# Performance work log

Hardware: AMD Instinct MI355X
Metric: run time of the kernel (lower is better)

## Reference

```python
import jax, jax.numpy as jnp
import numpy as np


def setup_inputs() -> dict:
    key = jax.random.key(0)
    k1, k2, k3, k4 = jax.random.split(key, 4)
    B, T, F_in, F_out, N, E, K = 16, 64, 64, 64, 128, 2, 4
    x = jax.random.normal(k1, (B, T, F_in, N), dtype=jnp.float32)
    # graph shift operator per (batch, time, edge-feature); scaled to keep powers bounded
    S = jax.random.normal(k2, (B, T, E, N, N), dtype=jnp.float32) / np.sqrt(N)
    H = jax.random.normal(k3, (F_out, E, K, F_in), dtype=jnp.float32) * 0.02
    bias = jax.random.normal(k4, (F_out, 1), dtype=jnp.float32) * 0.02
    return {"x": x, "S": S, "H": H, "bias": bias}


def reference(x, S, H, bias):
    # x: [B,T,F_in,N], S: [B,T,E,N,N], H: [F_out,E,K,F_in], bias: [F_out,1]
    B, T, F_in, N = x.shape
    E = S.shape[2]
    F_out, _, K, _ = H.shape
    # replicate features across edge-feature dim: [B,T,E,F_in,N]
    cur = jnp.broadcast_to(x[:, :, None], (B, T, E, F_in, N))
    taps = [cur]
    zero_row = jnp.zeros((B, 1, E, F_in, N), dtype=x.dtype)
    for _ in range(1, K):
        # time-shift: tap k at time t depends on tap k-1 at time t-1
        cur = jnp.concatenate([zero_row, cur[:, :-1]], axis=1)
        # diffuse over graph: [..,F_in,N] @ [..,N,N]
        cur = jnp.matmul(cur, S)
        taps.append(cur)
    z = jnp.stack(taps, axis=2)  # [B,T,K,E,F_in,N]
    # [B,T,N, E*K*F_in], matching permute(0,1,5,3,2,4) in the source
    z = z.transpose(0, 1, 5, 3, 2, 4).reshape(B, T, N, E * K * F_in)
    Hm = H.reshape(F_out, E * K * F_in)
    y = jnp.einsum('btnf,of->bton', z, Hm)  # [B,T,F_out,N]
    return y + bias  # bias [F_out,1] broadcasts over N
```

## Files before the change

kernel.cpp:

```cpp
#include <hip/hip_runtime.h>


namespace {
constexpr int B = 16, T = 64, F = 64, N = 128, E = 2, K = 4;
constexpr int SH = 72;
constexpr int SX = 72;
constexpr int SA = 136;
}

typedef short v8s __attribute__((ext_vector_type(8)));
typedef float v4f __attribute__((ext_vector_type(4)));

__device__ inline ushort f2bf(float f) {
  union { float f; uint u; } v; v.f = f;
  uint u = v.u;
  return (ushort)((u + 0x7fffu + ((u >> 16) & 1u)) >> 16);
}

__device__ inline uint4 pack8(const ushort* p) {
  uint4 w;
  w.x = (uint)p[0] | ((uint)p[1] << 16);
  w.y = (uint)p[2] | ((uint)p[3] << 16);
  w.z = (uint)p[4] | ((uint)p[5] << 16);
  w.w = (uint)p[6] | ((uint)p[7] << 16);
  return w;
}

__global__ __launch_bounds__(256) void cvt_S(const float* __restrict__ S,
                                             ushort* __restrict__ ST,
                                             int e_base, int e_count) {
  __shared__ ushort tile[128 * 130];
  const int bid = blockIdx.x;
  const int le = bid % e_count, s = (bid / e_count) % T, b = bid / (e_count * T);
  const int e = e_base + le;
  const float* Sg = S + (size_t)((b * T + s) * E + e) * N * N;
  ushort* Og = ST + (size_t)((b * T + s) * e_count + le) * N * N;
  const int tid = threadIdx.x;
  #pragma unroll
  for (int it = 0; it < 16; ++it) {
    const int idx = tid + it * 256;
    const int m = idx >> 5, n4 = (idx & 31) * 4;
    const float4 v = *(const float4*)(Sg + m * N + n4);
    uint* lp = (uint*)&tile[m * 130 + n4];
    lp[0] = (uint)f2bf(v.x) | ((uint)f2bf(v.y) << 16);
    lp[1] = (uint)f2bf(v.z) | ((uint)f2bf(v.w) << 16);
  }
  __syncthreads();
  #pragma unroll
  for (int it = 0; it < 4; ++it) {
    const int idx = tid + it * 256;
    const int m8 = (idx & 15) * 8, n2 = idx >> 4;
    uint r[8];
    #pragma unroll
    for (int j = 0; j < 8; ++j)
      r[j] = *(const uint*)&tile[(m8 + j) * 130 + 2 * n2];
    uint4 w0, w1;
    w0.x = (r[0] & 0xffffu) | (r[1] << 16);
    w0.y = (r[2] & 0xffffu) | (r[3] << 16);
    w0.z = (r[4] & 0xffffu) | (r[5] << 16);
    w0.w = (r[6] & 0xffffu) | (r[7] << 16);
    w1.x = (r[0] >> 16) | (r[1] & 0xffff0000u);
    w1.y = (r[2] >> 16) | (r[3] & 0xffff0000u);
    w1.z = (r[4] >> 16) | (r[5] & 0xffff0000u);
    w1.w = (r[6] >> 16) | (r[7] & 0xffff0000u);
    *(uint4*)(Og + (2 * n2) * N + m8) = w0;
    *(uint4*)(Og + (2 * n2 + 1) * N + m8) = w1;
  }
}

__device__ inline void stage_H(const float* __restrict__ Hg, int e, int k,
                               ushort* sH, int tid) {
  #pragma unroll
  for (int it = 0; it < 2; ++it) {
    const int idx = tid + it * 256;
    const int o = idx & 63, f8 = (idx >> 6) * 8;
    const float* src = Hg + ((size_t)(o * E + e) * K + k) * F + f8;
    ushort p[8];
    #pragma unroll
    for (int j = 0; j < 8; ++j) p[j] = f2bf(src[j]);
    *(uint4*)&sH[o * SH + f8] = pack8(p);
  }
}

__device__ inline void stage_X(const float* __restrict__ xg, ushort* sX, int tid) {
  #pragma unroll
  for (int it = 0; it < 4; ++it) {
    const int idx = tid + it * 256;
    const int n = idx & 127, f8 = (idx >> 7) * 8;
    ushort p[8];
    #pragma unroll
    for (int j = 0; j < 8; ++j) p[j] = f2bf(xg[(f8 + j) * N + n]);
    *(uint4*)&sX[n * SX + f8] = pack8(p);
  }
}

__device__ inline void stage_A(const ushort* __restrict__ Pg, ushort* sA, int tid) {
  #pragma unroll
  for (int it = 0; it < 4; ++it) {
    const int idx = tid + it * 256;
    const int o = idx >> 4, m8 = (idx & 15) * 8;
    *(uint4*)&sA[o * SA + m8] = *(const uint4*)(Pg + o * N + m8);
  }
}

__device__ inline void stage_Sh(const ushort* __restrict__ STg, int h,
                                ushort* sB, int tid) {
  #pragma unroll
  for (int it = 0; it < 4; ++it) {
    const int idx = tid + it * 256;
    const int n = idx >> 3, m8 = (idx & 7) * 8;
    *(uint4*)&sB[n * SX + m8] = *(const uint4*)(STg + n * N + h * 64 + m8);
  }
}

__device__ inline void zero_acc(v4f acc[2][4]) {
  #pragma unroll
  for (int i = 0; i < 2; ++i)
    #pragma unroll
    for (int j = 0; j < 4; ++j) {
      acc[i][j][0] = 0.f; acc[i][j][1] = 0.f; acc[i][j][2] = 0.f; acc[i][j][3] = 0.f;
    }
}

__device__ inline void do_proj(const ushort* sH, const ushort* sX, v4f acc[2][4],
                               int ob0, int nb0, int l15, int q) {
  #pragma unroll
  for (int fk = 0; fk < 2; ++fk) {
    v8s a[2], bb[4];
    #pragma unroll
    for (int mt = 0; mt < 2; ++mt)
      a[mt] = *(const v8s*)&sH[(ob0 + 16 * mt + l15) * SH + fk * 32 + q * 8];
    #pragma unroll
    for (int nt = 0; nt < 4; ++nt)
      bb[nt] = *(const v8s*)&sX[(nb0 + 16 * nt + l15) * SX + fk * 32 + q * 8];
    #pragma unroll
    for (int mt = 0; mt < 2; ++mt)
      #pragma unroll
      for (int nt = 0; nt < 4; ++nt)
        acc[mt][nt] = __builtin_amdgcn_mfma_f32_16x16x32_bf16(
            a[mt], bb[nt], acc[mt][nt], 0, 0, 0);
  }
}

__device__ inline void do_mm(const ushort* sA, const ushort* sB, int h,
                             v4f acc[2][4], int ob0, int nb0, int l15, int q) {
  #pragma unroll
  for (int lk = 0; lk < 2; ++lk) {
    v8s a[2], bb[4];
    #pragma unroll
    for (int mt = 0; mt < 2; ++mt)
      a[mt] = *(const v8s*)&sA[(ob0 + 16 * mt + l15) * SA + h * 64 + lk * 32 + q * 8];
    #pragma unroll
    for (int nt = 0; nt < 4; ++nt)
      bb[nt] = *(const v8s*)&sB[(nb0 + 16 * nt + l15) * SX + lk * 32 + q * 8];
    #pragma unroll
    for (int mt = 0; mt < 2; ++mt)
      #pragma unroll
      for (int nt = 0; nt < 4; ++nt)
        acc[mt][nt] = __builtin_amdgcn_mfma_f32_16x16x32_bf16(
            a[mt], bb[nt], acc[mt][nt], 0, 0, 0);
  }
}

__device__ inline void store_W(ushort* __restrict__ Wg, v4f acc[2][4],
                               int ob0, int nb0, int l15, int q) {
  #pragma unroll
  for (int mt = 0; mt < 2; ++mt)
    #pragma unroll
    for (int nt = 0; nt < 4; ++nt) {
      const int col = nb0 + 16 * nt + l15;
      #pragma unroll
      for (int r = 0; r < 4; ++r)
        Wg[(ob0 + 16 * mt + q * 4 + r) * N + col] = f2bf(acc[mt][nt][r]);
    }
}

__device__ inline void store_sA(ushort* sA, v4f acc[2][4],
                                int ob0, int nb0, int l15, int q) {
  #pragma unroll
  for (int mt = 0; mt < 2; ++mt)
    #pragma unroll
    for (int nt = 0; nt < 4; ++nt) {
      const int col = nb0 + 16 * nt + l15;
      #pragma unroll
      for (int r = 0; r < 4; ++r)
        sA[(ob0 + 16 * mt + q * 4 + r) * SA + col] = f2bf(acc[mt][nt][r]);
    }
}

__global__ __launch_bounds__(256) void gf_p2(
    const float* __restrict__ x, const ushort* __restrict__ ST,
    const float* __restrict__ H, ushort* __restrict__ Out,
    int e_base, int e_count) {
  __shared__ ushort sH[64 * SH];
  __shared__ ushort sB[128 * SX];
  __shared__ ushort sA[64 * SA];
  const int bid = blockIdx.x;
  const int le = bid % e_count, s = (bid / e_count) % T, b = bid / (e_count * T);
  const int e = e_base + le;
  const int tid = threadIdx.x, w = tid >> 6, lane = tid & 63;
  const int l15 = lane & 15, q = lane >> 4;
  const int ob0 = (w & 1) * 32, nb0 = (w >> 1) * 64;
  const bool has_p = (s > 0);
  const ushort* STg = ST + (size_t)((b * T + s) * e_count + le) * N * N;
  v4f acc[2][4];
  zero_acc(acc);
  if (has_p) {
    stage_H(H, e, 3, sH, tid);
    stage_X(x + (size_t)(b * T + s - 1) * F * N, sB, tid);
    __syncthreads();
    do_proj(sH, sB, acc, ob0, nb0, l15, q);
    __syncthreads();
    store_sA(sA, acc, ob0, nb0, l15, q);
    zero_acc(acc);
  }
  stage_H(H, e, 2, sH, tid);
  stage_X(x + (size_t)(b * T + s) * F * N, sB, tid);
  __syncthreads();
  do_proj(sH, sB, acc, ob0, nb0, l15, q);
  if (has_p) {
    #pragma unroll
    for (int h = 0; h < 2; ++h) {
      __syncthreads();
      stage_Sh(STg, h, sB, tid);
      __syncthreads();
      do_mm(sA, sB, h, acc, ob0, nb0, l15, q);
    }
  }
  store_W(Out + (size_t)((b * T + s) * e_count + le) * F * N, acc, ob0, nb0, l15, q);
}

__global__ __launch_bounds__(256) void gf_p1(
    const float* __restrict__ x, const ushort* __restrict__ ST,
    const float* __restrict__ H, const ushort* __restrict__ Pin,
    ushort* __restrict__ Out, int ktap, int e_base, int e_count) {
  __shared__ ushort sH[64 * SH];
  __shared__ ushort sB[128 * SX];
  __shared__ ushort sA[64 * SA];
  const int bid = blockIdx.x;
  const int le = bid % e_count, s = (bid / e_count) % T, b = bid / (e_count * T);
  const int e = e_base + le;
  const int tid = threadIdx.x, w = tid >> 6, lane = tid & 63;
  const int l15 = lane & 15, q = lane >> 4;
  const int ob0 = (w & 1) * 32, nb0 = (w >> 1) * 64;
  const bool has_p = (s > 0);
  const ushort* STg = ST + (size_t)((b * T + s) * e_count + le) * N * N;
  v4f acc[2][4];
  zero_acc(acc);
  stage_H(H, e, ktap, sH, tid);
  stage_X(x + (size_t)(b * T + s) * F * N, sB, tid);
  if (has_p)
    stage_A(Pin + (size_t)((b * T + s - 1) * e_count + le) * F * N, sA, tid);
  __syncthreads();
  do_proj(sH, sB, acc, ob0, nb0, l15, q);
  if (has_p) {
    #pragma unroll
    for (int h = 0; h < 2; ++h) {
      __syncthreads();
      stage_Sh(STg, h, sB, tid);
      __syncthreads();
      do_mm(sA, sB, h, acc, ob0, nb0, l15, q);
    }
  }
  store_W(Out + (size_t)((b * T + s) * e_count + le) * F * N, acc, ob0, nb0, l15, q);
}

__global__ __launch_bounds__(256) void gf_final(
    const float* __restrict__ x, const ushort* __restrict__ ST,
    const float* __restrict__ H, const float* __restrict__ bias,
    const ushort* __restrict__ Pin, float* __restrict__ y,
    int e_base, int e_count, int first_pass) {
  __shared__ ushort sH[64 * SH];
  __shared__ ushort sB[128 * SX];
  __shared__ ushort sA[64 * SA];
  const int bid = blockIdx.x;
  const int t = bid % T, b = bid / T;
  const int tid = threadIdx.x, w = tid >> 6, lane = tid & 63;
  const int l15 = lane & 15, q = lane >> 4;
  const int ob0 = (w & 1) * 32, nb0 = (w >> 1) * 64;
  const bool has_p = (t > 0);
  v4f acc[2][4];
  zero_acc(acc);
  for (int le = 0; le < e_count; ++le) {
    const int e = e_base + le;
    __syncthreads();
    stage_H(H, e, 0, sH, tid);
    stage_X(x + (size_t)(b * T + t) * F * N, sB, tid);
    if (has_p)
      stage_A(Pin + (size_t)((b * T + t - 1) * e_count + le) * F * N, sA, tid);
    __syncthreads();
    do_proj(sH, sB, acc, ob0, nb0, l15, q);
    if (has_p) {
      const ushort* STg = ST + (size_t)((b * T + t) * e_count + le) * N * N;
      #pragma unroll
      for (int h = 0; h < 2; ++h) {
        __syncthreads();
        stage_Sh(STg, h, sB, tid);
        __syncthreads();
        do_mm(sA, sB, h, acc, ob0, nb0, l15, q);
      }
    }
  }
  float* yg = y + (size_t)(b * T + t) * F * N;
  #pragma unroll
  for (int mt = 0; mt < 2; ++mt)
    #pragma unroll
    for (int nt = 0; nt < 4; ++nt) {
      const int col = nb0 + 16 * nt + l15;
      #pragma unroll
      for (int r = 0; r < 4; ++r) {
        const int row = ob0 + 16 * mt + q * 4 + r;
        float v = acc[mt][nt][r];
        v += first_pass ? bias[row] : yg[row * N + col];
        yg[row * N + col] = v;
      }
    }
}

extern "C" void kernel_launch(void* const* d_in, const int* in_sizes, int n_in,
                              void* d_out, int out_size, void* d_ws, size_t ws_size,
                              hipStream_t stream) {
  const float* x    = (const float*)d_in[0];
  const float* S    = (const float*)d_in[1];
  const float* H    = (const float*)d_in[2];
  const float* bias = (const float*)d_in[3];
  float* y = (float*)d_out;

  const size_t ST2 = (size_t)B * T * 2 * N * N;
  const size_t W2e = (size_t)B * T * 2 * F * N;
  const size_t need2 = (ST2 + 2 * W2e) * sizeof(ushort);

  if (ws_size >= need2) {
    ushort* ST   = (ushort*)d_ws;
    ushort* bufA = ST + ST2;
    ushort* bufB = bufA + W2e;
    cvt_S   <<<B * T * 2, 256, 0, stream>>>(S, ST, 0, 2);
    gf_p2   <<<B * T * 2, 256, 0, stream>>>(x, ST, H, bufA, 0, 2);
    gf_p1   <<<B * T * 2, 256, 0, stream>>>(x, ST, H, bufA, bufB, 1, 0, 2);
    gf_final<<<B * T,     256, 0, stream>>>(x, ST, H, bias, bufB, y, 0, 2, 1);
  } else {
    const size_t ST1 = (size_t)B * T * N * N;
    const size_t W1e = (size_t)B * T * F * N;
    ushort* ST   = (ushort*)d_ws;
    ushort* bufA = ST + ST1;
    ushort* bufB = bufA + W1e;
    for (int e = 0; e < E; ++e) {
      cvt_S   <<<B * T, 256, 0, stream>>>(S, ST, e, 1);
      gf_p2   <<<B * T, 256, 0, stream>>>(x, ST, H, bufA, e, 1);
      gf_p1   <<<B * T, 256, 0, stream>>>(x, ST, H, bufA, bufB, 1, e, 1);
      gf_final<<<B * T, 256, 0, stream>>>(x, ST, H, bias, bufB, y, e, 1, e == 0);
    }
  }
}
```

Before: 321.6 us.

## Fuse the three Horner-style filter passes into one kernel per output step

Replaces the p2/p1/final kernel chain with a single fused kernel in which each (b,t) block recomputes the chain for all taps and both edge features, keeping intermediates in shared memory and registers instead of writing bf16 buffers to global memory. H is converted to bf16 once by a small pre-kernel. This removes the intermediate global round-trips and two launches, but each block now redoes the projections for previous time steps and runs serially over both edge features with fewer blocks (B*T instead of B*T*2), which lowers parallelism.

```diff
diff --git a/kernel.cpp b/kernel.cpp
--- a/kernel.cpp
+++ b/kernel.cpp
@@ -26,15 +26,24 @@
   return w;
 }
 
+__global__ __launch_bounds__(256) void cvt_H(const float* __restrict__ H,
+                                             ushort* __restrict__ Hb) {
+  const int d4 = blockIdx.x * 256 + threadIdx.x;
+  const int d = d4 * 4;
+  const int f = d & 63, o = (d >> 6) & 63, k = (d >> 12) & 3, e = (d >> 14) & 1;
+  const float4 v = *(const float4*)(H + (((size_t)o * E + e) * K + k) * F + f);
+  uint2 w;
+  w.x = (uint)f2bf(v.x) | ((uint)f2bf(v.y) << 16);
+  w.y = (uint)f2bf(v.z) | ((uint)f2bf(v.w) << 16);
+  *(uint2*)(Hb + d) = w;
+}
+
 __global__ __launch_bounds__(256) void cvt_S(const float* __restrict__ S,
-                                             ushort* __restrict__ ST,
-                                             int e_base, int e_count) {
+                                             ushort* __restrict__ ST) {
   __shared__ ushort tile[128 * 130];
   const int bid = blockIdx.x;
-  const int le = bid % e_count, s = (bid / e_count) % T, b = bid / (e_count * T);
-  const int e = e_base + le;
-  const float* Sg = S + (size_t)((b * T + s) * E + e) * N * N;
-  ushort* Og = ST + (size_t)((b * T + s) * e_count + le) * N * N;
+  const float* Sg = S + (size_t)bid * N * N;
+  ushort* Og = ST + (size_t)bid * N * N;
   const int tid = threadIdx.x;
   #pragma unroll
   for (int it = 0; it < 16; ++it) {
@@ -68,21 +77,18 @@
   }
 }
 
-__device__ inline void stage_H(const float* __restrict__ Hg, int e, int k,
-                               ushort* sH, int tid) {
+__device__ inline void stage_Hb(const ushort* __restrict__ Hb, int e, int k,
+                                ushort* sH, int tid) {
+  const ushort* src = Hb + (size_t)((e * K + k) * 64) * 64;
   #pragma unroll
   for (int it = 0; it < 2; ++it) {
     const int idx = tid + it * 256;
-    const int o = idx & 63, f8 = (idx >> 6) * 8;
-    const float* src = Hg + ((size_t)(o * E + e) * K + k) * F + f8;
-    ushort p[8];
-    #pragma unroll
-    for (int j = 0; j < 8; ++j) p[j] = f2bf(src[j]);
-    *(uint4*)&sH[o * SH + f8] = pack8(p);
-  }
-}
-
-__device__ inline void stage_X(const float* __restrict__ xg, ushort* sX, int tid) {
+    const int o = idx >> 3, f8 = (idx & 7) * 8;
+    *(uint4*)&sH[o * SH + f8] = *(const uint4*)(src + o * 64 + f8);
+  }
+}
+
+__device__ inline void stage_X(const float* __restrict__ xg, ushort* sB, int tid) {
   #pragma unroll
   for (int it = 0; it < 4; ++it) {
     const int idx = tid + it * 256;
@@ -90,16 +96,7 @@
     ushort p[8];
     #pragma unroll
     for (int j = 0; j < 8; ++j) p[j] = f2bf(xg[(f8 + j) * N + n]);
-    *(uint4*)&sX[n * SX + f8] = pack8(p);
-  }
-}
-
-__device__ inline void stage_A(const ushort* __restrict__ Pg, ushort* sA, int tid) {
-  #pragma unroll
-  for (int it = 0; it < 4; ++it) {
-    const int idx = tid + it * 256;
-    const int o = idx >> 4, m8 = (idx & 15) * 8;
-    *(uint4*)&sA[o * SA + m8] = *(const uint4*)(Pg + o * N + m8);
+    *(uint4*)&sB[n * SX + f8] = pack8(p);
   }
 }
 
@@ -122,7 +119,7 @@
     }
 }
 
-__device__ inline void do_proj(const ushort* sH, const ushort* sX, v4f acc[2][4],
+__device__ inline void do_proj(const ushort* sH, const ushort* sB, v4f acc[2][4],
                                int ob0, int nb0, int l15, int q) {
   #pragma unroll
   for (int fk = 0; fk < 2; ++fk) {
@@ -132,7 +129,7 @@
       a[mt] = *(const v8s*)&sH[(ob0 + 16 * mt + l15) * SH + fk * 32 + q * 8];
     #pragma unroll
     for (int nt = 0; nt < 4; ++nt)
-      bb[nt] = *(const v8s*)&sX[(nb0 + 16 * nt + l15) * SX + fk * 32 + q * 8];
+      bb[nt] = *(const v8s*)&sB[(nb0 + 16 * nt + l15) * SX + fk * 32 + q * 8];
     #pragma unroll
     for (int mt = 0; mt < 2; ++mt)
       #pragma unroll
@@ -162,8 +159,8 @@
   }
 }
 
-__device__ inline void store_W(ushort* __restrict__ Wg, v4f acc[2][4],
-                               int ob0, int nb0, int l15, int q) {
+__device__ inline void store_sA(ushort* sA, v4f acc[2][4],
+                                int ob0, int nb0, int l15, int q) {
   #pragma unroll
   for (int mt = 0; mt < 2; ++mt)
     #pragma unroll
@@ -171,105 +168,14 @@
       const int col = nb0 + 16 * nt + l15;
       #pragma unroll
       for (int r = 0; r < 4; ++r)
-        Wg[(ob0 + 16 * mt + q * 4 + r) * N + col] = f2bf(acc[mt][nt][r]);
-    }
-}
-
-__device__ inline void store_sA(ushort* sA, v4f acc[2][4],
-                                int ob0, int nb0, int l15, int q) {
-  #pragma unroll
-  for (int mt = 0; mt < 2; ++mt)
-    #pragma unroll
-    for (int nt = 0; nt < 4; ++nt) {
-      const int col = nb0 + 16 * nt + l15;
-      #pragma unroll
-      for (int r = 0; r < 4; ++r)
         sA[(ob0 + 16 * mt + q * 4 + r) * SA + col] = f2bf(acc[mt][nt][r]);
     }
 }
 
-__global__ __launch_bounds__(256) void gf_p2(
+__global__ __launch_bounds__(256, 3) void gf_fused(
     const float* __restrict__ x, const ushort* __restrict__ ST,
-    const float* __restrict__ H, ushort* __restrict__ Out,
-    int e_base, int e_count) {
-  __shared__ ushort sH[64 * SH];
-  __shared__ ushort sB[128 * SX];
-  __shared__ ushort sA[64 * SA];
-  const int bid = blockIdx.x;
-  const int le = bid % e_count, s = (bid / e_count) % T, b = bid / (e_count * T);
-  const int e = e_base + le;
-  const int tid = threadIdx.x, w = tid >> 6, lane = tid & 63;
-  const int l15 = lane & 15, q = lane >> 4;
-  const int ob0 = (w & 1) * 32, nb0 = (w >> 1) * 64;
-  const bool has_p = (s > 0);
-  const ushort* STg = ST + (size_t)((b * T + s) * e_count + le) * N * N;
-  v4f acc[2][4];
-  zero_acc(acc);
-  if (has_p) {
-    stage_H(H, e, 3, sH, tid);
-    stage_X(x + (size_t)(b * T + s - 1) * F * N, sB, tid);
-    __syncthreads();
-    do_proj(sH, sB, acc, ob0, nb0, l15, q);
-    __syncthreads();
-    store_sA(sA, acc, ob0, nb0, l15, q);
-    zero_acc(acc);
-  }
-  stage_H(H, e, 2, sH, tid);
-  stage_X(x + (size_t)(b * T + s) * F * N, sB, tid);
-  __syncthreads();
-  do_proj(sH, sB, acc, ob0, nb0, l15, q);
-  if (has_p) {
-    #pragma unroll
-    for (int h = 0; h < 2; ++h) {
-      __syncthreads();
-      stage_Sh(STg, h, sB, tid);
-      __syncthreads();
-      do_mm(sA, sB, h, acc, ob0, nb0, l15, q);
-    }
-  }
-  store_W(Out + (size_t)((b * T + s) * e_count + le) * F * N, acc, ob0, nb0, l15, q);
-}
-
-__global__ __launch_bounds__(256) void gf_p1(
-    const float* __restrict__ x, const ushort* __restrict__ ST,
-    const float* __restrict__ H, const ushort* __restrict__ Pin,
-    ushort* __restrict__ Out, int ktap, int e_base, int e_count) {
-  __shared__ ushort sH[64 * SH];
-  __shared__ ushort sB[128 * SX];
-  __shared__ ushort sA[64 * SA];
-  const int bid = blockIdx.x;
-  const int le = bid % e_count, s = (bid / e_count) % T, b = bid / (e_count * T);
-  const int e = e_base + le;
-  const int tid = threadIdx.x, w = tid >> 6, lane = tid & 63;
-  const int l15 = lane & 15, q = lane >> 4;
-  const int ob0 = (w & 1) * 32, nb0 = (w >> 1) * 64;
-  const bool has_p = (s > 0);
-  const ushort* STg = ST + (size_t)((b * T + s) * e_count + le) * N * N;
-  v4f acc[2][4];
-  zero_acc(acc);
-  stage_H(H, e, ktap, sH, tid);
-  stage_X(x + (size_t)(b * T + s) * F * N, sB, tid);
-  if (has_p)
-    stage_A(Pin + (size_t)((b * T + s - 1) * e_count + le) * F * N, sA, tid);
-  __syncthreads();
-  do_proj(sH, sB, acc, ob0, nb0, l15, q);
-  if (has_p) {
-    #pragma unroll
-    for (int h = 0; h < 2; ++h) {
-      __syncthreads();
-      stage_Sh(STg, h, sB, tid);
-      __syncthreads();
-      do_mm(sA, sB, h, acc, ob0, nb0, l15, q);
-    }
-  }
-  store_W(Out + (size_t)((b * T + s) * e_count + le) * F * N, acc, ob0, nb0, l15, q);
-}
-
-__global__ __launch_bounds__(256) void gf_final(
-    const float* __restrict__ x, const ushort* __restrict__ ST,
-    const float* __restrict__ H, const float* __restrict__ bias,
-    const ushort* __restrict__ Pin, float* __restrict__ y,
-    int e_base, int e_count, int first_pass) {
+    const ushort* __restrict__ Hb, const float* __restrict__ bias,
+    float* __restrict__ y) {
   __shared__ ushort sH[64 * SH];
   __shared__ ushort sB[128 * SX];
   __shared__ ushort sA[64 * SA];
@@ -278,29 +184,45 @@
   const int tid = threadIdx.x, w = tid >> 6, lane = tid & 63;
   const int l15 = lane & 15, q = lane >> 4;
   const int ob0 = (w & 1) * 32, nb0 = (w >> 1) * 64;
-  const bool has_p = (t > 0);
+
+  v4f accY[2][4];
   v4f acc[2][4];
-  zero_acc(acc);
-  for (int le = 0; le < e_count; ++le) {
-    const int e = e_base + le;
-    __syncthreads();
-    stage_H(H, e, 0, sH, tid);
-    stage_X(x + (size_t)(b * T + t) * F * N, sB, tid);
-    if (has_p)
-      stage_A(Pin + (size_t)((b * T + t - 1) * e_count + le) * F * N, sA, tid);
-    __syncthreads();
-    do_proj(sH, sB, acc, ob0, nb0, l15, q);
-    if (has_p) {
-      const ushort* STg = ST + (size_t)((b * T + t) * e_count + le) * N * N;
-      #pragma unroll
-      for (int h = 0; h < 2; ++h) {
-        __syncthreads();
-        stage_Sh(STg, h, sB, tid);
-        __syncthreads();
-        do_mm(sA, sB, h, acc, ob0, nb0, l15, q);
+  zero_acc(accY);
+
+  for (int e = 0; e < E; ++e) {
+    bool have = false;
+    zero_acc(acc);
+    #pragma unroll
+    for (int k = 3; k >= 0; --k) {
+      const int s = t - k;
+      if (s < 0) continue;
+      const bool prevP = have;
+      __syncthreads();
+      if (prevP) store_sA(sA, acc, ob0, nb0, l15, q);
+      stage_Hb(Hb, e, k, sH, tid);
+      stage_X(x + (size_t)(b * T + s) * F * N, sB, tid);
+      __syncthreads();
+      if (k == 0) {
+        do_proj(sH, sB, accY, ob0, nb0, l15, q);
+      } else {
+        zero_acc(acc);
+        do_proj(sH, sB, acc, ob0, nb0, l15, q);
       }
-    }
-  }
+      if (prevP) {
+        const ushort* STg = ST + (size_t)((b * T + s) * E + e) * N * N;
+        #pragma unroll
+        for (int h = 0; h < 2; ++h) {
+          __syncthreads();
+          stage_Sh(STg, h, sB, tid);
+          __syncthreads();
+          if (k == 0) do_mm(sA, sB, h, accY, ob0, nb0, l15, q);
+          else        do_mm(sA, sB, h, acc,  ob0, nb0, l15, q);
+        }
+      }
+      have = true;
+    }
+  }
+
   float* yg = y + (size_t)(b * T + t) * F * N;
   #pragma unroll
   for (int mt = 0; mt < 2; ++mt)
@@ -310,9 +232,7 @@
       #pragma unroll
       for (int r = 0; r < 4; ++r) {
         const int row = ob0 + 16 * mt + q * 4 + r;
-        float v = acc[mt][nt][r];
-        v += first_pass ? bias[row] : yg[row * N + col];
-        yg[row * N + col] = v;
+        yg[row * N + col] = accY[mt][nt][r] + bias[row];
       }
     }
 }
@@ -326,29 +246,11 @@
   const float* bias = (const float*)d_in[3];
   float* y = (float*)d_out;
 
-  const size_t ST2 = (size_t)B * T * 2 * N * N;
-  const size_t W2e = (size_t)B * T * 2 * F * N;
-  const size_t need2 = (ST2 + 2 * W2e) * sizeof(ushort);
-
-  if (ws_size >= need2) {
-    ushort* ST   = (ushort*)d_ws;
-    ushort* bufA = ST + ST2;
-    ushort* bufB = bufA + W2e;
-    cvt_S   <<<B * T * 2, 256, 0, stream>>>(S, ST, 0, 2);
-    gf_p2   <<<B * T * 2, 256, 0, stream>>>(x, ST, H, bufA, 0, 2);
-    gf_p1   <<<B * T * 2, 256, 0, stream>>>(x, ST, H, bufA, bufB, 1, 0, 2);
-    gf_final<<<B * T,     256, 0, stream>>>(x, ST, H, bias, bufB, y, 0, 2, 1);
-  } else {
-    const size_t ST1 = (size_t)B * T * N * N;
-    const size_t W1e = (size_t)B * T * F * N;
-    ushort* ST   = (ushort*)d_ws;
-    ushort* bufA = ST + ST1;
-    ushort* bufB = bufA + W1e;
-    for (int e = 0; e < E; ++e) {
-      cvt_S   <<<B * T, 256, 0, stream>>>(S, ST, e, 1);
-      gf_p2   <<<B * T, 256, 0, stream>>>(x, ST, H, bufA, e, 1);
-      gf_p1   <<<B * T, 256, 0, stream>>>(x, ST, H, bufA, bufB, 1, e, 1);
-      gf_final<<<B * T, 256, 0, stream>>>(x, ST, H, bias, bufB, y, e, 1, e == 0);
-    }
-  }
-}
+  const size_t STn = (size_t)B * T * E * N * N;
+  ushort* ST = (ushort*)d_ws;
+  ushort* Hb = ST + STn;
+
+  cvt_H   <<<32,        256, 0, stream>>>(H, Hb);
+  cvt_S   <<<B * T * E, 256, 0, stream>>>(S, ST);
+  gf_fused<<<B * T,     256, 0, stream>>>(x, ST, Hb, bias, y);
+}
```

Result: slower. 332.0 us (+3.2%).
